# Kernel optimization log

Hardware: AMD Instinct MI355X
Metric: run time of the kernel (lower is better)

## Reference

```python
import jax, jax.numpy as jnp
import numpy as np

N_NODES = 65536
N_EDGES = 1048576


def gcn_conv(x, W, b, src, dst, n_nodes):
    """PyG GCNConv (normalize=True, add_self_loops already applied in src/dst):
    out = D^{-1/2} (A+I) D^{-1/2} X W + b, aggregated at dst (target) nodes."""
    deg = jax.ops.segment_sum(jnp.ones_like(dst, dtype=x.dtype), dst, num_segments=n_nodes)
    dis = jax.lax.rsqrt(jnp.maximum(deg, 1.0))  # self loops guarantee deg >= 1
    norm = dis[src] * dis[dst]                  # [E]
    h = x @ W                                   # [N, out]
    agg = jax.ops.segment_sum(h[src] * norm[:, None], dst, num_segments=n_nodes)
    return agg + b


def setup_inputs() -> dict:
    key = jax.random.key(0)
    ks = jax.random.split(key, 8)
    x = jax.random.normal(ks[0], (N_NODES, 128), dtype=jnp.float32)
    edge_index = jax.random.randint(ks[1], (2, N_EDGES), 0, N_NODES, dtype=jnp.int64)
    dims = [(128, 256), (256, 128), (128, 64)]
    params = {}
    for i, (din, dout) in enumerate(dims):
        scale = 1.0 / np.sqrt(din)
        params[f"W{i+1}"] = jax.random.uniform(ks[2 + i], (din, dout), dtype=jnp.float32, minval=-scale, maxval=scale)
        params[f"b{i+1}"] = jnp.zeros((dout,), dtype=jnp.float32)
    return {"x": x, "edge_index": edge_index, **params}


def reference(x, edge_index, W1, b1, W2, b2, W3, b3):
    n = x.shape[0]
    loop = jnp.arange(n, dtype=edge_index.dtype)
    src = jnp.concatenate([edge_index[0], loop])  # add self loops
    dst = jnp.concatenate([edge_index[1], loop])
    for W, b in ((W1, b1), (W2, b2), (W3, b3)):
        x = gcn_conv(x, W, b, src, dst, n)
        x = jax.nn.softmax(jax.nn.relu(x), axis=1)  # ReLU then Softmax(dim=1) per layer
    return x
```

## Files before the change

### kernel.cpp

```cpp
#include <hip/hip_runtime.h>
#include <cstdint>
#include <cstddef>

#define N_NODES 65536
#define N_EDGES 1048576
#define E_TOT   (N_EDGES + N_NODES)
#define CAP     5120

using short8  = __attribute__((ext_vector_type(8))) short;
using floatx4 = __attribute__((ext_vector_type(4))) float;
using half8   = __attribute__((ext_vector_type(8))) _Float16;
using half4   = __attribute__((ext_vector_type(4))) _Float16;
typedef unsigned short ushort_t;

__device__ inline void split_bf16(float a, short& hi, short& lo) {
    unsigned u  = __float_as_uint(a);
    unsigned hr = (u + 0x7fffu + ((u >> 16) & 1u)) >> 16;
    float    hf = __uint_as_float(hr << 16);
    hi = (short)hr;
    float    lf = a - hf;
    lo = (short)(__float_as_uint(lf) >> 16);
}


__global__ __launch_bounds__(1024) void k_bucket(const int* __restrict__ src, const int* __restrict__ dst,
                                                 int* __restrict__ gcur, unsigned* __restrict__ pk) {
    __shared__ int cnt[256];
    __shared__ int cur[256];
    int tid = threadIdx.x;
    if (tid < 256) cnt[tid] = 0;
    __syncthreads();
    int base = blockIdx.x * 4096;
    #pragma unroll
    for (int j = 0; j < 4; ++j) {
        int d = __builtin_nontemporal_load(&dst[base + j * 1024 + tid]);
        atomicAdd(&cnt[d >> 8], 1);
    }
    __syncthreads();
    if (tid < 256) cur[tid] = CAP * tid + atomicAdd(&gcur[tid], cnt[tid]);
    __syncthreads();
    #pragma unroll
    for (int j = 0; j < 4; ++j) {
        int e = base + j * 1024 + tid;
        int d = __builtin_nontemporal_load(&dst[e]);
        int s = __builtin_nontemporal_load(&src[e]);
        int pos = atomicAdd(&cur[d >> 8], 1);
        pk[pos] = ((unsigned)s << 16) | (unsigned)d;
    }
}

__global__ __launch_bounds__(256) void k_boff(const int* __restrict__ gcur, int* __restrict__ boff,
                                              int* __restrict__ off) {
    __shared__ int sb[256];
    int tid = threadIdx.x;
    int v = gcur[tid] + 256;
    sb[tid] = v;
    __syncthreads();
    #pragma unroll
    for (int s = 1; s < 256; s <<= 1) {
        int t = (tid >= s) ? sb[tid - s] : 0;
        __syncthreads();
        sb[tid] += t;
        __syncthreads();
    }
    boff[tid] = sb[tid] - v;
    if (tid == 255) boff[256] = sb[255];
    if (tid == 0) off[N_NODES] = E_TOT;
}

__global__ __launch_bounds__(1024) void k_sortb(const unsigned* __restrict__ pk, const int* __restrict__ gcur,
                                                const int* __restrict__ boff, int* __restrict__ off,
                                                float* __restrict__ dis, ushort_t* __restrict__ ssort) {
    __shared__ int cnt[256];
    __shared__ int sb[256];
    __shared__ int cur[256];
    int b = blockIdx.x;
    int tid = threadIdx.x;
    int n = gcur[b];
    const unsigned* p = pk + (size_t)b * CAP;
    if (tid < 256) cnt[tid] = 0;
    __syncthreads();
    for (int i = tid; i < n; i += 1024) atomicAdd(&cnt[p[i] & 255u], 1);
    __syncthreads();
    if (tid < 256) sb[tid] = cnt[tid];
    __syncthreads();
    #pragma unroll
    for (int s = 1; s < 256; s <<= 1) {
        int t = (tid < 256 && tid >= s) ? sb[tid - s] : 0;
        __syncthreads();
        if (tid < 256) sb[tid] += t;
        __syncthreads();
    }
    if (tid < 256) {
        int deg = cnt[tid];
        int o = boff[b] + (sb[tid] - deg) + tid;
        int d = b * 256 + tid;
        off[d] = o;
        dis[d] = rsqrtf((float)(deg + 1));
        ssort[o + deg] = (ushort_t)d;
        cur[tid] = o;
    }
    __syncthreads();
    for (int i = tid; i < n; i += 1024) {
        unsigned v = p[i];
        int pos = atomicAdd(&cur[v & 255u], 1);
        ssort[pos] = (ushort_t)(v >> 16);
    }
}


#define G1 (16 * 4 * 64)
#define G2 (8 * 8 * 64)
#define G3 (4 * 4 * 64)
#define NBX 8192
#define NBW ((G1 + G2 + G3 + 255) / 256)

__device__ inline void convw_split(const float* W, int K, int N, short* Bh, short* Bl, int g) {
    int lane = g & 63;
    int kt = (g >> 6) % (K / 32);
    int nt = (g >> 6) / (K / 32);
    int n = nt * 16 + (lane & 15);
    int kbase = kt * 32 + (lane >> 4) * 8;
    #pragma unroll
    for (int j = 0; j < 8; ++j) {
        short h, l;
        split_bf16(W[(size_t)(kbase + j) * N + n], h, l);
        Bh[(size_t)g * 8 + j] = h;
        Bl[(size_t)g * 8 + j] = l;
    }
}

__device__ inline void convw_h(const float* W, int K, int N, _Float16* Bf, int g) {
    int lane = g & 63;
    int kt = (g >> 6) % (K / 32);
    int nt = (g >> 6) / (K / 32);
    int n = nt * 16 + (lane & 15);
    int kbase = kt * 32 + (lane >> 4) * 8;
    #pragma unroll
    for (int j = 0; j < 8; ++j)
        Bf[(size_t)g * 8 + j] = (_Float16)W[(size_t)(kbase + j) * N + n];
}

__global__ __launch_bounds__(256) void k_fused(
        const float* __restrict__ x, const float* __restrict__ dis, _Float16* __restrict__ xh,
        const float* __restrict__ W1, short* __restrict__ w1h, short* __restrict__ w1l,
        const float* __restrict__ W2, _Float16* __restrict__ w2f,
        const float* __restrict__ W3, _Float16* __restrict__ w3f) {
    int b = blockIdx.x;
    if (b < NBX) {
        int idx = (b * 256 + threadIdx.x) * 4;
        int row = idx >> 7;
        float d = dis[row];
        float4 v = *(const float4*)(x + idx);
        half4 o = {(_Float16)(d * v.x), (_Float16)(d * v.y), (_Float16)(d * v.z), (_Float16)(d * v.w)};
        *(half4*)(xh + idx) = o;
    } else {
        int g = (b - NBX) * 256 + threadIdx.x;
        if (g < G1)                 convw_split(W1, 128, 256, w1h, w1l, g);
        else if (g < G1 + G2)       convw_h(W2, 256, 128, w2f, g - G1);
        else if (g < G1 + G2 + G3)  convw_h(W3, 128, 64, w3f, g - G1 - G2);
    }
}


__global__ __launch_bounds__(256) void k_l12(const _Float16* __restrict__ A,
        const short* __restrict__ Bh, const short* __restrict__ Bl,
        const float* __restrict__ b1,
        const _Float16* __restrict__ w2f,
        const float* __restrict__ dis, _Float16* __restrict__ hh) {
    constexpr int NT1 = 16;
    constexpr int KT1 = 4;
    constexpr int KT2 = 8;
    constexpr int NT2 = 8;
    constexpr int LSTR = 272;
    __shared__ __align__(16) _Float16 xt[4][16][LSTR];

    int tid = threadIdx.x;
    int wave = tid >> 6, lane = tid & 63;
    int quad = lane >> 4, li = lane & 15;
    size_t row0 = (size_t)blockIdx.x * 64;
    const _Float16* ap = A + (row0 + wave * 16 + li) * 128 + quad * 8;

    floatx4 acc[NT1];
    #pragma unroll
    for (int t = 0; t < NT1; ++t) acc[t] = (floatx4)0.0f;

    #pragma unroll
    for (int kt = 0; kt < KT1; ++kt) {
        half8 a8 = *(const half8*)(ap + kt * 32);
        short ah[8], al[8];
        #pragma unroll
        for (int j = 0; j < 8; ++j) split_bf16((float)a8[j], ah[j], al[j]);
        short8 afh = *(short8*)ah;
        short8 afl = *(short8*)al;
        #pragma unroll
        for (int nt = 0; nt < NT1; ++nt) {
            size_t bi = ((size_t)(nt * KT1 + kt) * 64 + lane);
            short8 bfh = ((const short8*)Bh)[bi];
            short8 bfl = ((const short8*)Bl)[bi];
            acc[nt] = __builtin_amdgcn_mfma_f32_16x16x32_bf16(bfh, afh, acc[nt], 0, 0, 0);
            acc[nt] = __builtin_amdgcn_mfma_f32_16x16x32_bf16(bfl, afh, acc[nt], 0, 0, 0);
            acc[nt] = __builtin_amdgcn_mfma_f32_16x16x32_bf16(bfh, afl, acc[nt], 0, 0, 0);
        }
    }

    float mr = 0.0f;
    #pragma unroll
    for (int nt = 0; nt < NT1; ++nt) {
        float4 bv = *(const float4*)(b1 + nt * 16 + quad * 4);
        float bb[4] = {bv.x, bv.y, bv.z, bv.w};
        #pragma unroll
        for (int r = 0; r < 4; ++r) {
            float v = fmaxf(acc[nt][r] + bb[r], 0.0f);
            acc[nt][r] = v;
            mr = fmaxf(mr, v);
        }
    }
    mr = fmaxf(mr, __shfl_xor(mr, 16, 64));
    mr = fmaxf(mr, __shfl_xor(mr, 32, 64));
    float sum = 0.0f;
    #pragma unroll
    for (int nt = 0; nt < NT1; ++nt)
        #pragma unroll
        for (int r = 0; r < 4; ++r) {
            float t = __expf(acc[nt][r] - mr);
            acc[nt][r] = t;
            sum += t;
        }
    sum += __shfl_xor(sum, 16, 64);
    sum += __shfl_xor(sum, 32, 64);
    float inv = 1.0f / sum;

    _Float16* xrow = &xt[wave][li][0];
    #pragma unroll
    for (int nt = 0; nt < NT1; ++nt) {
        half4 h4 = {(_Float16)(acc[nt][0] * inv), (_Float16)(acc[nt][1] * inv),
                    (_Float16)(acc[nt][2] * inv), (_Float16)(acc[nt][3] * inv)};
        *(half4*)(xrow + nt * 16 + quad * 4) = h4;
    }
    __syncthreads();

    floatx4 acc2[NT2];
    #pragma unroll
    for (int t = 0; t < NT2; ++t) acc2[t] = (floatx4)0.0f;
    #pragma unroll
    for (int kt = 0; kt < KT2; ++kt) {
        half8 a8 = *(const half8*)(xrow + kt * 32 + quad * 8);
        #pragma unroll
        for (int nt = 0; nt < NT2; ++nt) {
            half8 bf = ((const half8*)w2f)[(size_t)(nt * KT2 + kt) * 64 + lane];
            acc2[nt] = __builtin_amdgcn_mfma_f32_16x16x32_f16(a8, bf, acc2[nt], 0, 0, 0);
        }
    }
    size_t rbase = row0 + wave * 16 + quad * 4;
    float4 d4 = *(const float4*)(dis + rbase);
    float dr[4] = {d4.x, d4.y, d4.z, d4.w};
    #pragma unroll
    for (int nt = 0; nt < NT2; ++nt)
        #pragma unroll
        for (int r = 0; r < 4; ++r)
            hh[(rbase + r) * 128 + nt * 16 + li] = (_Float16)(acc2[nt][r] * dr[r]);
}


template <int K, int N>
__global__ __launch_bounds__(256) void k_mmh(const _Float16* __restrict__ A,
                                             const _Float16* __restrict__ Bf,
                                             const float* __restrict__ dis, _Float16* __restrict__ Cout) {
    constexpr int NT = N / 16;
    constexpr int KT = K / 32;
    int tid = threadIdx.x;
    int wave = tid >> 6, lane = tid & 63;
    int quad = lane >> 4, col = lane & 15;
    size_t row0 = (size_t)blockIdx.x * 64;
    const _Float16* ap = A + (row0 + wave * 16 + col) * K + quad * 8;

    floatx4 acc[NT];
    #pragma unroll
    for (int t = 0; t < NT; ++t) acc[t] = (floatx4)0.0f;

    for (int kt = 0; kt < KT; ++kt) {
        half8 a8 = *(const half8*)(ap + kt * 32);
        #pragma unroll
        for (int nt = 0; nt < NT; ++nt) {
            half8 bf = ((const half8*)Bf)[(size_t)(nt * KT + kt) * 64 + lane];
            acc[nt] = __builtin_amdgcn_mfma_f32_16x16x32_f16(a8, bf, acc[nt], 0, 0, 0);
        }
    }

    size_t rbase = row0 + wave * 16 + quad * 4;
    float4 d4 = *(const float4*)(dis + rbase);
    float dr[4] = {d4.x, d4.y, d4.z, d4.w};
    #pragma unroll
    for (int nt = 0; nt < NT; ++nt)
        #pragma unroll
        for (int r = 0; r < 4; ++r)
            Cout[(rbase + r) * N + nt * 16 + col] = (_Float16)(acc[nt][r] * dr[r]);
}


template <int LPN, bool ACT, typename OutT>
__global__ __launch_bounds__(256) void k_aggq(const _Float16* __restrict__ h, const int* __restrict__ off,
                                              const ushort_t* __restrict__ ss, const float* __restrict__ dis,
                                              const float* __restrict__ bias, OutT* __restrict__ out) {
    constexpr int D = LPN * 8;
    constexpr int NPW = 64 / LPN;
    int lane = threadIdx.x & 63;
    int grp  = lane / LPN;
    int li   = lane & (LPN - 1);
    int c0   = li * 8;
    int n = (blockIdx.x * 4 + (threadIdx.x >> 6)) * NPW + grp;
    int e0 = off[n], e1 = off[n + 1];

    const _Float16* hb = h + c0;

    half8 hacc = {0, 0, 0, 0, 0, 0, 0, 0};
    half8 hacc2 = {0, 0, 0, 0, 0, 0, 0, 0};
    float facc[8];
    #pragma unroll
    for (int j = 0; j < 8; ++j) facc[j] = 0.0f;

    int e = e0;
    for (; e + 8 <= e1; e += 8) {
        int s0 = ss[e];
        int s1 = ss[e + 1];
        int s2 = ss[e + 2];
        int s3 = ss[e + 3];
        int s4 = ss[e + 4];
        int s5 = ss[e + 5];
        int s6 = ss[e + 6];
        int s7 = ss[e + 7];
        half8 v0 = *(const half8*)(hb + (size_t)s0 * D);
        half8 v1 = *(const half8*)(hb + (size_t)s1 * D);
        half8 v2 = *(const half8*)(hb + (size_t)s2 * D);
        half8 v3 = *(const half8*)(hb + (size_t)s3 * D);
        half8 v4 = *(const half8*)(hb + (size_t)s4 * D);
        half8 v5 = *(const half8*)(hb + (size_t)s5 * D);
        half8 v6 = *(const half8*)(hb + (size_t)s6 * D);
        half8 v7 = *(const half8*)(hb + (size_t)s7 * D);
        half8 p0 = (v0 + v1) + (v2 + v3);
        half8 p1 = (v4 + v5) + (v6 + v7);
        if constexpr (ACT) {
            hacc  += p0;
            hacc2 += p1;
        } else {
            #pragma unroll
            for (int j = 0; j < 8; ++j) facc[j] += (float)p0[j];
            #pragma unroll
            for (int j = 0; j < 8; ++j) facc[j] += (float)p1[j];
        }
    }
    for (; e + 4 <= e1; e += 4) {
        int s0 = ss[e];
        int s1 = ss[e + 1];
        int s2 = ss[e + 2];
        int s3 = ss[e + 3];
        half8 v0 = *(const half8*)(hb + (size_t)s0 * D);
        half8 v1 = *(const half8*)(hb + (size_t)s1 * D);
        half8 v2 = *(const half8*)(hb + (size_t)s2 * D);
        half8 v3 = *(const half8*)(hb + (size_t)s3 * D);
        half8 p = (v0 + v1) + (v2 + v3);
        if constexpr (ACT) {
            hacc += p;
        } else {
            #pragma unroll
            for (int j = 0; j < 8; ++j) facc[j] += (float)p[j];
        }
    }
    int rem = e1 - e;
    if (rem > 0) {
        int s0 = ss[e];
        half8 p = *(const half8*)(hb + (size_t)s0 * D);
        if (rem > 1) {
            int s1 = ss[e + 1];
            p += *(const half8*)(hb + (size_t)s1 * D);
        }
        if (rem > 2) {
            int s2 = ss[e + 2];
            p += *(const half8*)(hb + (size_t)s2 * D);
        }
        if constexpr (ACT) {
            hacc += p;
        } else {
            #pragma unroll
            for (int j = 0; j < 8; ++j) facc[j] += (float)p[j];
        }
    }
    if constexpr (ACT) {
        hacc += hacc2;
        #pragma unroll
        for (int j = 0; j < 8; ++j) facc[j] = (float)hacc[j];
    }

    float dn = dis[n];
    if constexpr (ACT) {
        float m = 0.0f;
        #pragma unroll
        for (int j = 0; j < 8; ++j) {
            float v = fmaxf(fmaf(facc[j], dn, bias[c0 + j]), 0.0f);
            facc[j] = v;
            m = fmaxf(m, v);
        }
        #pragma unroll
        for (int mask = LPN / 2; mask > 0; mask >>= 1) m = fmaxf(m, __shfl_xor(m, mask, 64));
        float sum = 0.0f;
        #pragma unroll
        for (int j = 0; j < 8; ++j) {
            float t = __expf(facc[j] - m);
            facc[j] = t;
            sum += t;
        }
        #pragma unroll
        for (int mask = LPN / 2; mask > 0; mask >>= 1) sum += __shfl_xor(sum, mask, 64);
        float inv = 1.0f / sum;
        #pragma unroll
        for (int j = 0; j < 8; ++j) facc[j] *= inv;
    } else {
        #pragma unroll
        for (int j = 0; j < 8; ++j) facc[j] *= dn;
    }

    if constexpr (sizeof(OutT) == 2) {
        half8 o;
        #pragma unroll
        for (int j = 0; j < 8; ++j) o[j] = (_Float16)facc[j];
        *(half8*)((_Float16*)out + (size_t)n * D + c0) = o;
    } else {
        float* op = (float*)out + (size_t)n * D + c0;
        *(float4*)(op)     = make_float4(facc[0], facc[1], facc[2], facc[3]);
        *(float4*)(op + 4) = make_float4(facc[4], facc[5], facc[6], facc[7]);
    }
}


extern "C" void kernel_launch(void* const* d_in, const int* in_sizes, int n_in,
                              void* d_out, int out_size, void* d_ws, size_t ws_size,
                              hipStream_t stream) {
    const float* x  = (const float*)d_in[0];
    const int*   ei = (const int*)d_in[1];
    const float* W1 = (const float*)d_in[2];
    const float* b1 = (const float*)d_in[3];
    const float* W2 = (const float*)d_in[4];
    const float* b2 = (const float*)d_in[5];
    const float* W3 = (const float*)d_in[6];
    const float* b3 = (const float*)d_in[7];
    const int* srcE = ei;
    const int* dstE = ei + N_EDGES;

    char* p = (char*)d_ws;
    auto carve = [&](size_t bytes) {
        char* q = p;
        p += (bytes + 255) & ~(size_t)255;
        return q;
    };
    int*          gcur  = (int*)carve(sizeof(int) * 256);
    int*          boff  = (int*)carve(sizeof(int) * 257);
    int*          off   = (int*)carve(sizeof(int) * (N_NODES + 1));
    float*        dis   = (float*)carve(sizeof(float) * N_NODES);
    unsigned*     pk    = (unsigned*)carve(sizeof(unsigned) * 256 * CAP);
    ushort_t*     ssort = (ushort_t*)carve(sizeof(ushort_t) * E_TOT);
    short*        w1h   = (short*)carve(sizeof(short) * 128 * 256);
    short*        w1l   = (short*)carve(sizeof(short) * 128 * 256);
    _Float16*     w2f   = (_Float16*)carve(sizeof(_Float16) * 256 * 128);
    _Float16*     w3f   = (_Float16*)carve(sizeof(_Float16) * 128 * 64);
    _Float16*     xh    = (_Float16*)carve(sizeof(_Float16) * (size_t)N_NODES * 128);
    _Float16*     a0h   = (_Float16*)carve(sizeof(_Float16) * (size_t)N_NODES * 128);
    _Float16*     x2h   = (_Float16*)carve(sizeof(_Float16) * (size_t)N_NODES * 128);
    _Float16*     hh    = (_Float16*)carve(sizeof(_Float16) * (size_t)N_NODES * 128);

    (void)hipMemsetAsync(gcur, 0, sizeof(int) * 256, stream);
    k_bucket<<<256, 1024, 0, stream>>>(srcE, dstE, gcur, pk);
    k_boff<<<1, 256, 0, stream>>>(gcur, boff, off);
    k_sortb<<<256, 1024, 0, stream>>>(pk, gcur, boff, off, dis, ssort);
    k_fused<<<NBX + NBW, 256, 0, stream>>>(x, dis, xh, W1, w1h, w1l, W2, w2f, W3, w3f);

    k_aggq<16, false, _Float16><<<N_NODES / 16, 256, 0, stream>>>(xh, off, ssort, dis, nullptr, a0h);
    k_l12<<<N_NODES / 64, 256, 0, stream>>>(a0h, w1h, w1l, b1, w2f, dis, hh);
    k_aggq<16, true, _Float16><<<N_NODES / 16, 256, 0, stream>>>(hh, off, ssort, dis, b2, x2h);
    k_mmh<128, 64><<<N_NODES / 64, 256, 0, stream>>>(x2h, w3f, dis, hh);
    k_aggq<8, true, float><<<N_NODES / 32, 256, 0, stream>>>(hh, off, ssort, dis, b3, (float*)d_out);
}
```

Before: 261.9 us.

## Split fused layer-1/2 GEMM across waves by output columns with cross-wave softmax

Reassigns work in the fused layer-1/layer-2 kernel so each wave computes a 64-column slice for all 64 rows of the block, instead of all columns for 16 rows. Each weight fragment loaded from global memory is now reused across four row tiles, which cuts per-wave weight traffic. The row softmax now has to combine partial max and sum values across waves through shared memory. That adds two block barriers and a larger shared tile that every wave reads for the second GEMM.

```diff
diff --git a/kernel.cpp b/kernel.cpp
--- a/kernel.cpp
+++ b/kernel.cpp
@@ -168,98 +168,148 @@
         const float* __restrict__ b1,
         const _Float16* __restrict__ w2f,
         const float* __restrict__ dis, _Float16* __restrict__ hh) {
-    constexpr int NT1 = 16;
-    constexpr int KT1 = 4;
-    constexpr int KT2 = 8;
-    constexpr int NT2 = 8;
-    constexpr int LSTR = 272;
-    __shared__ __align__(16) _Float16 xt[4][16][LSTR];
+    constexpr int LSTR = 280;
+    __shared__ __align__(16) _Float16 xt[64][LSTR];
+    __shared__ float red[2][4][64];
 
     int tid = threadIdx.x;
-    int wave = tid >> 6, lane = tid & 63;
+    int w = tid >> 6, lane = tid & 63;
     int quad = lane >> 4, li = lane & 15;
     size_t row0 = (size_t)blockIdx.x * 64;
-    const _Float16* ap = A + (row0 + wave * 16 + li) * 128 + quad * 8;
-
-    floatx4 acc[NT1];
-    #pragma unroll
-    for (int t = 0; t < NT1; ++t) acc[t] = (floatx4)0.0f;
-
-    #pragma unroll
-    for (int kt = 0; kt < KT1; ++kt) {
-        half8 a8 = *(const half8*)(ap + kt * 32);
-        short ah[8], al[8];
-        #pragma unroll
-        for (int j = 0; j < 8; ++j) split_bf16((float)a8[j], ah[j], al[j]);
-        short8 afh = *(short8*)ah;
-        short8 afl = *(short8*)al;
-        #pragma unroll
-        for (int nt = 0; nt < NT1; ++nt) {
-            size_t bi = ((size_t)(nt * KT1 + kt) * 64 + lane);
+
+    floatx4 acc[4][4];
+    #pragma unroll
+    for (int ntl = 0; ntl < 4; ++ntl)
+        #pragma unroll
+        for (int rt = 0; rt < 4; ++rt) acc[ntl][rt] = (floatx4)0.0f;
+
+    #pragma unroll
+    for (int kt = 0; kt < 4; ++kt) {
+        short8 afh[4], afl[4];
+        #pragma unroll
+        for (int rt = 0; rt < 4; ++rt) {
+            half8 a8 = *(const half8*)(A + (row0 + rt * 16 + li) * 128 + kt * 32 + quad * 8);
+            short ah[8], al[8];
+            #pragma unroll
+            for (int j = 0; j < 8; ++j) split_bf16((float)a8[j], ah[j], al[j]);
+            afh[rt] = *(short8*)ah;
+            afl[rt] = *(short8*)al;
+        }
+        #pragma unroll
+        for (int ntl = 0; ntl < 4; ++ntl) {
+            size_t bi = ((size_t)((w * 4 + ntl) * 4 + kt) * 64 + lane);
             short8 bfh = ((const short8*)Bh)[bi];
             short8 bfl = ((const short8*)Bl)[bi];
-            acc[nt] = __builtin_amdgcn_mfma_f32_16x16x32_bf16(bfh, afh, acc[nt], 0, 0, 0);
-            acc[nt] = __builtin_amdgcn_mfma_f32_16x16x32_bf16(bfl, afh, acc[nt], 0, 0, 0);
-            acc[nt] = __builtin_amdgcn_mfma_f32_16x16x32_bf16(bfh, afl, acc[nt], 0, 0, 0);
-        }
-    }
-
-    float mr = 0.0f;
-    #pragma unroll
-    for (int nt = 0; nt < NT1; ++nt) {
-        float4 bv = *(const float4*)(b1 + nt * 16 + quad * 4);
-        float bb[4] = {bv.x, bv.y, bv.z, bv.w};
-        #pragma unroll
-        for (int r = 0; r < 4; ++r) {
-            float v = fmaxf(acc[nt][r] + bb[r], 0.0f);
-            acc[nt][r] = v;
-            mr = fmaxf(mr, v);
-        }
-    }
-    mr = fmaxf(mr, __shfl_xor(mr, 16, 64));
-    mr = fmaxf(mr, __shfl_xor(mr, 32, 64));
-    float sum = 0.0f;
-    #pragma unroll
-    for (int nt = 0; nt < NT1; ++nt)
-        #pragma unroll
-        for (int r = 0; r < 4; ++r) {
-            float t = __expf(acc[nt][r] - mr);
-            acc[nt][r] = t;
-            sum += t;
-        }
-    sum += __shfl_xor(sum, 16, 64);
-    sum += __shfl_xor(sum, 32, 64);
-    float inv = 1.0f / sum;
-
-    _Float16* xrow = &xt[wave][li][0];
-    #pragma unroll
-    for (int nt = 0; nt < NT1; ++nt) {
-        half4 h4 = {(_Float16)(acc[nt][0] * inv), (_Float16)(acc[nt][1] * inv),
-                    (_Float16)(acc[nt][2] * inv), (_Float16)(acc[nt][3] * inv)};
-        *(half4*)(xrow + nt * 16 + quad * 4) = h4;
-    }
-    __syncthreads();
-
-    floatx4 acc2[NT2];
-    #pragma unroll
-    for (int t = 0; t < NT2; ++t) acc2[t] = (floatx4)0.0f;
-    #pragma unroll
-    for (int kt = 0; kt < KT2; ++kt) {
-        half8 a8 = *(const half8*)(xrow + kt * 32 + quad * 8);
-        #pragma unroll
-        for (int nt = 0; nt < NT2; ++nt) {
-            half8 bf = ((const half8*)w2f)[(size_t)(nt * KT2 + kt) * 64 + lane];
-            acc2[nt] = __builtin_amdgcn_mfma_f32_16x16x32_f16(a8, bf, acc2[nt], 0, 0, 0);
-        }
-    }
-    size_t rbase = row0 + wave * 16 + quad * 4;
-    float4 d4 = *(const float4*)(dis + rbase);
-    float dr[4] = {d4.x, d4.y, d4.z, d4.w};
-    #pragma unroll
-    for (int nt = 0; nt < NT2; ++nt)
-        #pragma unroll
-        for (int r = 0; r < 4; ++r)
-            hh[(rbase + r) * 128 + nt * 16 + li] = (_Float16)(acc2[nt][r] * dr[r]);
+            #pragma unroll
+            for (int rt = 0; rt < 4; ++rt) {
+                acc[ntl][rt] = __builtin_amdgcn_mfma_f32_16x16x32_bf16(bfh, afh[rt], acc[ntl][rt], 0, 0, 0);
+                acc[ntl][rt] = __builtin_amdgcn_mfma_f32_16x16x32_bf16(bfl, afh[rt], acc[ntl][rt], 0, 0, 0);
+                acc[ntl][rt] = __builtin_amdgcn_mfma_f32_16x16x32_bf16(bfh, afl[rt], acc[ntl][rt], 0, 0, 0);
+            }
+        }
+    }
+
+    float bb[4][4];
+    #pragma unroll
+    for (int ntl = 0; ntl < 4; ++ntl) {
+        float4 bv = *(const float4*)(b1 + w * 64 + ntl * 16 + quad * 4);
+        bb[ntl][0] = bv.x; bb[ntl][1] = bv.y; bb[ntl][2] = bv.z; bb[ntl][3] = bv.w;
+    }
+    float mr[4] = {0.f, 0.f, 0.f, 0.f};
+    #pragma unroll
+    for (int ntl = 0; ntl < 4; ++ntl)
+        #pragma unroll
+        for (int rt = 0; rt < 4; ++rt)
+            #pragma unroll
+            for (int r = 0; r < 4; ++r) {
+                float v = fmaxf(acc[ntl][rt][r] + bb[ntl][r], 0.0f);
+                acc[ntl][rt][r] = v;
+                mr[rt] = fmaxf(mr[rt], v);
+            }
+    #pragma unroll
+    for (int rt = 0; rt < 4; ++rt) {
+        mr[rt] = fmaxf(mr[rt], __shfl_xor(mr[rt], 16, 64));
+        mr[rt] = fmaxf(mr[rt], __shfl_xor(mr[rt], 32, 64));
+    }
+    {
+        float wv = (quad == 0) ? mr[0] : (quad == 1) ? mr[1] : (quad == 2) ? mr[2] : mr[3];
+        red[0][w][quad * 16 + li] = wv;
+    }
+    __syncthreads();
+    float m[4];
+    #pragma unroll
+    for (int rt = 0; rt < 4; ++rt) {
+        int idx = rt * 16 + li;
+        m[rt] = fmaxf(fmaxf(red[0][0][idx], red[0][1][idx]), fmaxf(red[0][2][idx], red[0][3][idx]));
+    }
+    float sr[4] = {0.f, 0.f, 0.f, 0.f};
+    #pragma unroll
+    for (int ntl = 0; ntl < 4; ++ntl)
+        #pragma unroll
+        for (int rt = 0; rt < 4; ++rt)
+            #pragma unroll
+            for (int r = 0; r < 4; ++r) {
+                float t = __expf(acc[ntl][rt][r] - m[rt]);
+                acc[ntl][rt][r] = t;
+                sr[rt] += t;
+            }
+    #pragma unroll
+    for (int rt = 0; rt < 4; ++rt) {
+        sr[rt] += __shfl_xor(sr[rt], 16, 64);
+        sr[rt] += __shfl_xor(sr[rt], 32, 64);
+    }
+    {
+        float sv = (quad == 0) ? sr[0] : (quad == 1) ? sr[1] : (quad == 2) ? sr[2] : sr[3];
+        red[1][w][quad * 16 + li] = sv;
+    }
+    __syncthreads();
+    float inv[4];
+    #pragma unroll
+    for (int rt = 0; rt < 4; ++rt) {
+        int idx = rt * 16 + li;
+        inv[rt] = 1.0f / (red[1][0][idx] + red[1][1][idx] + red[1][2][idx] + red[1][3][idx]);
+    }
+    #pragma unroll
+    for (int ntl = 0; ntl < 4; ++ntl)
+        #pragma unroll
+        for (int rt = 0; rt < 4; ++rt) {
+            half4 h4 = {(_Float16)(acc[ntl][rt][0] * inv[rt]), (_Float16)(acc[ntl][rt][1] * inv[rt]),
+                        (_Float16)(acc[ntl][rt][2] * inv[rt]), (_Float16)(acc[ntl][rt][3] * inv[rt])};
+            *(half4*)(&xt[rt * 16 + li][w * 64 + ntl * 16 + quad * 4]) = h4;
+        }
+    __syncthreads();
+
+    floatx4 acc2[2][4];
+    #pragma unroll
+    for (int ntl2 = 0; ntl2 < 2; ++ntl2)
+        #pragma unroll
+        for (int rt = 0; rt < 4; ++rt) acc2[ntl2][rt] = (floatx4)0.0f;
+
+    #pragma unroll
+    for (int kt = 0; kt < 8; ++kt) {
+        half8 a8[4];
+        #pragma unroll
+        for (int rt = 0; rt < 4; ++rt)
+            a8[rt] = *(const half8*)(&xt[rt * 16 + li][kt * 32 + quad * 8]);
+        #pragma unroll
+        for (int ntl2 = 0; ntl2 < 2; ++ntl2) {
+            half8 bf = ((const half8*)w2f)[(size_t)((w * 2 + ntl2) * 8 + kt) * 64 + lane];
+            #pragma unroll
+            for (int rt = 0; rt < 4; ++rt)
+                acc2[ntl2][rt] = __builtin_amdgcn_mfma_f32_16x16x32_f16(a8[rt], bf, acc2[ntl2][rt], 0, 0, 0);
+        }
+    }
+    #pragma unroll
+    for (int rt = 0; rt < 4; ++rt) {
+        size_t rbase = row0 + rt * 16 + quad * 4;
+        float4 d4 = *(const float4*)(dis + rbase);
+        float dr[4] = {d4.x, d4.y, d4.z, d4.w};
+        #pragma unroll
+        for (int ntl2 = 0; ntl2 < 2; ++ntl2)
+            #pragma unroll
+            for (int r = 0; r < 4; ++r)
+                hh[(rbase + r) * 128 + (w * 2 + ntl2) * 16 + li] = (_Float16)(acc2[ntl2][rt][r] * dr[r]);
+    }
 }
 
 
```

Result: faster. 254.2 us (-2.9%).
